# Optimization experiments

Hardware: AMD Instinct MI355X
Metric: run time of the kernel (lower is better)

Reference implementation:

```python
import jax, jax.numpy as jnp
import numpy as np

N_NODES = 50000
N_EDGES = 640000
DIM = 128
N_LAYERS = 4
K_MAX = 4


def setup_inputs() -> dict:
    key = jax.random.key(0)
    k1, k2, k3, k4, k5, k6 = jax.random.split(key, 6)
    x = jax.random.normal(k1, (N_NODES, DIM), dtype=jnp.float32)
    edge_index = jax.random.randint(k2, (2, N_EDGES), 0, N_NODES, dtype=jnp.int32)
    edge_attr = jax.random.randint(k3, (N_EDGES,), 1, K_MAX + 1, dtype=jnp.int32)  # hop k in [1, k_max]
    W = jax.random.normal(k4, (N_LAYERS, DIM, DIM), dtype=jnp.float32) * 0.05
    b = jax.random.normal(k5, (N_LAYERS, DIM), dtype=jnp.float32) * 0.01
    alpha = jax.random.normal(k6, (N_LAYERS, K_MAX), dtype=jnp.float32)
    return {"x": x, "edge_index": edge_index, "edge_attr": edge_attr,
            "W": W, "b": b, "alpha": alpha}


def reference(x, edge_index, edge_attr, W, b, alpha):
    # SP-GCN stage: per-hop GCN convs with shared per-layer weight W[t],
    # combined with softmax(alpha[t]) hop weights, residual + ReLU + L2 norm.
    N, D = x.shape
    L, K = alpha.shape
    src, dst = edge_index[0], edge_index[1]
    k_idx = edge_attr - 1                              # [E] in [0, K)

    # Per-(node, hop) in-degree with self-loop (+1), as in gcn_norm per k-subgraph.
    seg = dst * K + k_idx
    ones = jnp.ones(src.shape[0], dtype=x.dtype)
    deg = jax.ops.segment_sum(ones, seg, num_segments=N * K).reshape(N, K) + 1.0  # [N, K]
    dinv = jax.lax.rsqrt(deg)
    # symmetric norm per edge within its hop-k subgraph
    norm_e = dinv[src, k_idx] * dinv[dst, k_idx]       # [E]

    for t in range(L):
        a = jax.nn.softmax(alpha[t])                   # [K] hop weights
        h = x @ W[t]                                   # [N, D]
        # sum_k alpha_k * conv_k fused: per-edge weight alpha[k_e] * norm_e
        msg = (a[k_idx] * norm_e)[:, None] * h[src]    # [E, D]
        agg = jax.ops.segment_sum(msg, dst, num_segments=N)
        # self-loop contributions: sum_k alpha_k / deg[n, k]
        self_coef = jnp.sum(a[None, :] / deg, axis=1)  # [N]
        out = agg + self_coef[:, None] * h + b[t]
        x = x + jax.nn.relu(out)
        # F.normalize(p=2, dim=-1), eps=1e-12
        nrm = jnp.maximum(jnp.linalg.norm(x, axis=-1, keepdims=True), 1e-12)
        x = x / nrm
    return x
```

## Files before the change

### kernel.cpp

```cpp
#include <hip/hip_runtime.h>
#include <hip/hip_fp16.h>
#include <math.h>

#define DIM 128
#define KH 4

typedef unsigned int uint;
typedef unsigned short ushort;

__global__ __launch_bounds__(256) void k_init(const float4* __restrict__ xin,
                                              float4* __restrict__ X4,
                                              uint* __restrict__ degpack,
                                              int n4, int N) {
  int i = blockIdx.x * 256 + threadIdx.x;
  if (i < n4) X4[i] = xin[i];
  if (i < N) degpack[i] = 0;
}

__global__ __launch_bounds__(256) void k_count(const int* __restrict__ ei,
                                               const int* __restrict__ attr,
                                               uint* __restrict__ degpack, int E) {
  int e = blockIdx.x * 256 + threadIdx.x;
  if (e >= E) return;
  int dst = ei[E + e];
  int k = attr[e] - 1;
  atomicAdd(&degpack[dst], 1u << (k * 8));
}

__global__ __launch_bounds__(256) void k_scan1(const uint* __restrict__ degpack,
                                               int* __restrict__ off,
                                               int* __restrict__ bsum, int n) {
  __shared__ int s[256];
  int t = threadIdx.x;
  int i = blockIdx.x * 256 + t;
  int v = 0;
  if (i < n) {
    uint w = degpack[i];
    v = (w & 0xff) + ((w >> 8) & 0xff) + ((w >> 16) & 0xff) + (w >> 24);
  }
  s[t] = v;
  __syncthreads();
  for (int d = 1; d < 256; d <<= 1) {
    int u = (t >= d) ? s[t - d] : 0;
    __syncthreads();
    s[t] += u;
    __syncthreads();
  }
  if (i < n) off[i] = s[t] - v;
  if (t == 255) bsum[blockIdx.x] = s[255];
}

__global__ __launch_bounds__(256) void k_scan2(const int* __restrict__ bsum,
                                               int* __restrict__ bex, int nb) {
  __shared__ int s[256];
  int t = threadIdx.x;
  int v = (t < nb) ? bsum[t] : 0;
  s[t] = v;
  __syncthreads();
  for (int d = 1; d < 256; d <<= 1) {
    int u = (t >= d) ? s[t - d] : 0;
    __syncthreads();
    s[t] += u;
    __syncthreads();
  }
  if (t < nb) bex[t] = s[t] - v;
}

__global__ __launch_bounds__(256) void k_scan3(int* __restrict__ off,
                                               const int* __restrict__ bex,
                                               const uint* __restrict__ degpack,
                                               int* __restrict__ cursor4,
                                               float* __restrict__ dinv, int n) {
  int i = blockIdx.x * 256 + threadIdx.x;
  if (i >= n) return;
  int o = off[i] + bex[blockIdx.x];
  off[i] = o;
  uint w = degpack[i];
  int b0 = w & 0xff, b1 = (w >> 8) & 0xff, b2 = (w >> 16) & 0xff, b3 = w >> 24;
  int4 c;
  c.x = o;
  c.y = o + b0;
  c.z = o + b0 + b1;
  c.w = o + b0 + b1 + b2;
  *(int4*)&cursor4[i * 4] = c;
  float4 dv;
  dv.x = rsqrtf((float)b0 + 1.0f);
  dv.y = rsqrtf((float)b1 + 1.0f);
  dv.z = rsqrtf((float)b2 + 1.0f);
  dv.w = rsqrtf((float)b3 + 1.0f);
  *(float4*)&dinv[i * 4] = dv;
}

__global__ __launch_bounds__(256) void k_scatter(const int* __restrict__ ei,
                                                 const int* __restrict__ attr,
                                                 const float* __restrict__ dinv,
                                                 int* __restrict__ cursor4,
                                                 uint* __restrict__ srcnm, int E) {
  int e = blockIdx.x * 256 + threadIdx.x;
  if (e >= E) return;
  int src = ei[e];
  int dst = ei[E + e];
  int k = attr[e] - 1;
  float nm = dinv[src * KH + k] * dinv[dst * KH + k];
  ushort h = __half_as_ushort(__float2half(nm));
  int pos = atomicAdd(&cursor4[dst * KH + k], 1);
  srcnm[pos] = (uint)src | ((uint)h << 16);
}

__device__ __forceinline__ uint f2bf(float f) {
  uint u = __float_as_uint(f);
  return (u + 0x7fffu + ((u >> 16) & 1u)) >> 16;
}
__device__ __forceinline__ float bflo(uint u) { return __uint_as_float(u << 16); }
__device__ __forceinline__ float bfhi(uint u) { return __uint_as_float(u & 0xffff0000u); }

#define FMA4(A, xc, wv)                 \
  A.x = fmaf(xc, wv.x, A.x);            \
  A.y = fmaf(xc, wv.y, A.y);            \
  A.z = fmaf(xc, wv.z, A.z);            \
  A.w = fmaf(xc, wv.w, A.w);

__global__ __launch_bounds__(256) void k_gemm(const float* __restrict__ X,
                                              const float* __restrict__ W,
                                              uint* __restrict__ Hb,
                                              int N) {
  __shared__ float xs[64][64];
  __shared__ float ws[64][128];
  int t = threadIdx.x;
  int r0 = blockIdx.x * 64;
  int tc = t & 31;
  int tr = t >> 5;
  float4 acc[8];
#pragma unroll
  for (int i = 0; i < 8; ++i) acc[i] = make_float4(0.f, 0.f, 0.f, 0.f);

  for (int kb = 0; kb < 2; ++kb) {
    __syncthreads();
#pragma unroll
    for (int i = 0; i < 4; ++i) {
      int fi = i * 256 + t;
      int kq = fi & 15, rr = fi >> 4;
      int row = r0 + rr;
      if (row >= N) row = N - 1;
      *(float4*)&xs[rr][kq * 4] =
          *(const float4*)&X[(size_t)row * DIM + kb * 64 + kq * 4];
    }
#pragma unroll
    for (int i = 0; i < 8; ++i) {
      int fi = i * 256 + t;
      int jq = fi & 31, kk = fi >> 5;
      *(float4*)&ws[kk][jq * 4] =
          *(const float4*)&W[(size_t)(kb * 64 + kk) * DIM + jq * 4];
    }
    __syncthreads();
#pragma unroll
    for (int k4 = 0; k4 < 16; ++k4) {
      float4 wv0 = *(float4*)&ws[k4 * 4 + 0][tc * 4];
      float4 wv1 = *(float4*)&ws[k4 * 4 + 1][tc * 4];
      float4 wv2 = *(float4*)&ws[k4 * 4 + 2][tc * 4];
      float4 wv3 = *(float4*)&ws[k4 * 4 + 3][tc * 4];
#pragma unroll
      for (int rr = 0; rr < 8; ++rr) {
        float4 xv = *(float4*)&xs[tr * 8 + rr][k4 * 4];
        FMA4(acc[rr], xv.x, wv0)
        FMA4(acc[rr], xv.y, wv1)
        FMA4(acc[rr], xv.z, wv2)
        FMA4(acc[rr], xv.w, wv3)
      }
    }
  }
#pragma unroll
  for (int rr = 0; rr < 8; ++rr) {
    int row = r0 + tr * 8 + rr;
    if (row < N) {
      uint2 o;
      o.x = f2bf(acc[rr].x) | (f2bf(acc[rr].y) << 16);
      o.y = f2bf(acc[rr].z) | (f2bf(acc[rr].w) << 16);
      *(uint2*)&Hb[(size_t)row * 64 + tc * 2] = o;
    }
  }
}

__global__ __launch_bounds__(256) void k_agg(const int* __restrict__ off,
                                             const uint* __restrict__ degpack,
                                             const uint* __restrict__ srcnm,
                                             const float* __restrict__ dinv,
                                             const uint* __restrict__ Hb,
                                             const float* __restrict__ bias,
                                             const float* __restrict__ alpha,
                                             float* __restrict__ X, int N) {
  int wid = threadIdx.x >> 6;
  int lane = threadIdx.x & 63;
  int n = blockIdx.x * 4 + wid;
  if (n >= N) return;

  float a0 = alpha[0], a1 = alpha[1], a2 = alpha[2], a3 = alpha[3];
  float m = fmaxf(fmaxf(a0, a1), fmaxf(a2, a3));
  a0 = __expf(a0 - m); a1 = __expf(a1 - m); a2 = __expf(a2 - m); a3 = __expf(a3 - m);
  float is = 1.0f / (a0 + a1 + a2 + a3);
  a0 *= is; a1 *= is; a2 *= is; a3 *= is;

  uint w = degpack[n];
  int b0 = w & 0xff, b1 = (w >> 8) & 0xff, b2 = (w >> 16) & 0xff, b3 = (int)(w >> 24);
  int e0 = off[n];
  int e1 = e0 + b0 + b1 + b2 + b3;
  int k1 = e0 + b0, k2 = k1 + b1, k3 = k2 + b2;

  float accx = 0.f, accy = 0.f;

  for (int base = e0; base < e1; base += 64) {
    int cnt = min(64, e1 - base);
    int sofs = 0;
    float wc = 0.f;
    if (lane < cnt) {
      uint v = srcnm[base + lane];
      int pos = base + lane;
      int k = (pos >= k1) + (pos >= k2) + (pos >= k3);
      float ak = (k == 0) ? a0 : (k == 1) ? a1 : (k == 2) ? a2 : a3;
      wc = ak * __half2float(__ushort_as_half((ushort)(v >> 16)));
      sofs = (int)(v & 0xFFFFu) << 6;
    }
    int j = 0;
    for (; j + 4 <= cnt; j += 4) {
      int s0 = __shfl(sofs, j),     s1 = __shfl(sofs, j + 1);
      int s2 = __shfl(sofs, j + 2), s3 = __shfl(sofs, j + 3);
      float w0 = __shfl(wc, j),     w1 = __shfl(wc, j + 1);
      float w2 = __shfl(wc, j + 2), w3 = __shfl(wc, j + 3);
      uint u0 = Hb[s0 + lane];
      uint u1 = Hb[s1 + lane];
      uint u2 = Hb[s2 + lane];
      uint u3 = Hb[s3 + lane];
      accx = fmaf(w0, bflo(u0), accx); accy = fmaf(w0, bfhi(u0), accy);
      accx = fmaf(w1, bflo(u1), accx); accy = fmaf(w1, bfhi(u1), accy);
      accx = fmaf(w2, bflo(u2), accx); accy = fmaf(w2, bfhi(u2), accy);
      accx = fmaf(w3, bflo(u3), accx); accy = fmaf(w3, bfhi(u3), accy);
    }
    for (; j < cnt; ++j) {
      int sj = __shfl(sofs, j);
      float wj = __shfl(wc, j);
      uint uj = Hb[sj + lane];
      accx = fmaf(wj, bflo(uj), accx);
      accy = fmaf(wj, bfhi(uj), accy);
    }
  }

  float4 dv = *(const float4*)&dinv[n * 4];
  float sc = a0 * dv.x * dv.x + a1 * dv.y * dv.y + a2 * dv.z * dv.z + a3 * dv.w * dv.w;

  uint un = Hb[(size_t)n * 64 + lane];
  float2 bb = ((const float2*)bias)[lane];
  float2 xo = ((const float2*)X)[(size_t)n * 64 + lane];
  float o0 = accx + sc * bflo(un) + bb.x;
  float o1 = accy + sc * bfhi(un) + bb.y;
  float x0 = xo.x + fmaxf(o0, 0.f);
  float x1 = xo.y + fmaxf(o1, 0.f);

  float ss = x0 * x0 + x1 * x1;
#pragma unroll
  for (int d = 32; d; d >>= 1) ss += __shfl_xor(ss, d);
  float nrm = fmaxf(sqrtf(ss), 1e-12f);
  float inv = 1.0f / nrm;
  ((float2*)X)[(size_t)n * 64 + lane] = make_float2(x0 * inv, x1 * inv);
}

extern "C" void kernel_launch(void* const* d_in, const int* in_sizes, int n_in,
                              void* d_out, int out_size, void* d_ws, size_t ws_size,
                              hipStream_t stream) {
  const float* x = (const float*)d_in[0];
  const int* ei = (const int*)d_in[1];
  const int* attr = (const int*)d_in[2];
  const float* W = (const float*)d_in[3];
  const float* b = (const float*)d_in[4];
  const float* alpha = (const float*)d_in[5];
  float* X = (float*)d_out;

  int N = in_sizes[0] / DIM;
  int E = in_sizes[1] / 2;
  int L = in_sizes[3] / (DIM * DIM);

  char* base = (char*)d_ws;
  size_t ofs = 0;
  auto carve = [&](size_t bytes) -> void* {
    void* p = base + ofs;
    ofs = (ofs + bytes + 255) & ~(size_t)255;
    return p;
  };
  int* off = (int*)carve((size_t)(N + 1) * 4);
  int* cursor4 = (int*)carve((size_t)N * KH * 4);
  uint* degpack = (uint*)carve((size_t)N * 4);
  float* dinv = (float*)carve((size_t)N * KH * 4);
  int* bsum = (int*)carve(256 * 4);
  int* bex = (int*)carve(256 * 4);
  uint* srcnm = (uint*)carve((size_t)E * 4);
  uint* Hb = (uint*)carve((size_t)N * 64 * 4);

  int n4 = N * DIM / 4;
  int nb = (N + 255) / 256;

  k_init<<<(n4 + 255) / 256, 256, 0, stream>>>((const float4*)x, (float4*)X,
                                               degpack, n4, N);
  k_count<<<(E + 255) / 256, 256, 0, stream>>>(ei, attr, degpack, E);
  k_scan1<<<nb, 256, 0, stream>>>(degpack, off, bsum, N);
  k_scan2<<<1, 256, 0, stream>>>(bsum, bex, nb);
  k_scan3<<<nb, 256, 0, stream>>>(off, bex, degpack, cursor4, dinv, N);
  k_scatter<<<(E + 255) / 256, 256, 0, stream>>>(ei, attr, dinv, cursor4, srcnm, E);

  for (int t = 0; t < L; ++t) {
    k_gemm<<<(N + 63) / 64, 256, 0, stream>>>(X, W + (size_t)t * DIM * DIM, Hb, N);
    k_agg<<<(N + 3) / 4, 256, 0, stream>>>(off, degpack, srcnm, dinv, Hb,
                                           b + (size_t)t * DIM, alpha + (size_t)t * KH,
                                           X, N);
  }
}
```

Baseline: 334.4 us.

## Replace FP32 FMA GEMM with split-bf16 MFMA GEMM using hi/lo operands

```diff
diff --git a/kernel.cpp b/kernel.cpp
--- a/kernel.cpp
+++ b/kernel.cpp
@@ -7,14 +7,53 @@
 
 typedef unsigned int uint;
 typedef unsigned short ushort;
+using short8v = __attribute__((ext_vector_type(8))) short;
+using f32x4 = __attribute__((ext_vector_type(4))) float;
+
+__device__ __forceinline__ uint f2bf(float f) {
+  uint u = __float_as_uint(f);
+  return (u + 0x7fffu + ((u >> 16) & 1u)) >> 16;
+}
+__device__ __forceinline__ float bf2f(uint u) { return __uint_as_float(u << 16); }
+__device__ __forceinline__ float bflo(uint u) { return __uint_as_float(u << 16); }
+__device__ __forceinline__ float bfhi(uint u) { return __uint_as_float(u & 0xffff0000u); }
 
 __global__ __launch_bounds__(256) void k_init(const float4* __restrict__ xin,
                                               float4* __restrict__ X4,
+                                              uint* __restrict__ Xhi,
+                                              uint* __restrict__ Xlo,
                                               uint* __restrict__ degpack,
                                               int n4, int N) {
   int i = blockIdx.x * 256 + threadIdx.x;
-  if (i < n4) X4[i] = xin[i];
+  if (i < n4) {
+    float4 v = xin[i];
+    X4[i] = v;
+    uint h0 = f2bf(v.x), h1 = f2bf(v.y), h2 = f2bf(v.z), h3 = f2bf(v.w);
+    Xhi[i * 2 + 0] = h0 | (h1 << 16);
+    Xhi[i * 2 + 1] = h2 | (h3 << 16);
+    uint l0 = f2bf(v.x - bf2f(h0)), l1 = f2bf(v.y - bf2f(h1));
+    uint l2 = f2bf(v.z - bf2f(h2)), l3 = f2bf(v.w - bf2f(h3));
+    Xlo[i * 2 + 0] = l0 | (l1 << 16);
+    Xlo[i * 2 + 1] = l2 | (l3 << 16);
+  }
   if (i < N) degpack[i] = 0;
+}
+
+__global__ __launch_bounds__(256) void k_wprep(const float* __restrict__ W,
+                                               short* __restrict__ Whi,
+                                               short* __restrict__ Wlo, int total) {
+  int idx = blockIdx.x * 256 + threadIdx.x;
+  if (idx >= total) return;
+  int l = idx >> 14;
+  int rem = idx & 16383;
+  int k = rem >> 7;
+  int n = rem & 127;
+  float w = W[idx];
+  uint h = f2bf(w);
+  uint lo = f2bf(w - bf2f(h));
+  size_t o = (size_t)l * 16384 + (size_t)n * 128 + k;
+  Whi[o] = (short)h;
+  Wlo[o] = (short)lo;
 }
 
 __global__ __launch_bounds__(256) void k_count(const int* __restrict__ ei,
@@ -107,78 +146,77 @@
   srcnm[pos] = (uint)src | ((uint)h << 16);
 }
 
-__device__ __forceinline__ uint f2bf(float f) {
-  uint u = __float_as_uint(f);
-  return (u + 0x7fffu + ((u >> 16) & 1u)) >> 16;
-}
-__device__ __forceinline__ float bflo(uint u) { return __uint_as_float(u << 16); }
-__device__ __forceinline__ float bfhi(uint u) { return __uint_as_float(u & 0xffff0000u); }
-
-#define FMA4(A, xc, wv)                 \
-  A.x = fmaf(xc, wv.x, A.x);            \
-  A.y = fmaf(xc, wv.y, A.y);            \
-  A.z = fmaf(xc, wv.z, A.z);            \
-  A.w = fmaf(xc, wv.w, A.w);
-
-__global__ __launch_bounds__(256) void k_gemm(const float* __restrict__ X,
-                                              const float* __restrict__ W,
-                                              uint* __restrict__ Hb,
-                                              int N) {
-  __shared__ float xs[64][64];
-  __shared__ float ws[64][128];
+__global__ __launch_bounds__(512) void k_gemm(const uint* __restrict__ Xhi,
+                                              const uint* __restrict__ Xlo,
+                                              const short* __restrict__ Whi,
+                                              const short* __restrict__ Wlo,
+                                              ushort* __restrict__ Hb16, int N) {
+  __shared__ __align__(16) short xs_hi[64 * 128];
+  __shared__ __align__(16) short xs_lo[64 * 128];
   int t = threadIdx.x;
   int r0 = blockIdx.x * 64;
-  int tc = t & 31;
-  int tr = t >> 5;
-  float4 acc[8];
-#pragma unroll
-  for (int i = 0; i < 8; ++i) acc[i] = make_float4(0.f, 0.f, 0.f, 0.f);
-
-  for (int kb = 0; kb < 2; ++kb) {
-    __syncthreads();
-#pragma unroll
-    for (int i = 0; i < 4; ++i) {
-      int fi = i * 256 + t;
-      int kq = fi & 15, rr = fi >> 4;
-      int row = r0 + rr;
-      if (row >= N) row = N - 1;
-      *(float4*)&xs[rr][kq * 4] =
-          *(const float4*)&X[(size_t)row * DIM + kb * 64 + kq * 4];
-    }
-#pragma unroll
-    for (int i = 0; i < 8; ++i) {
-      int fi = i * 256 + t;
-      int jq = fi & 31, kk = fi >> 5;
-      *(float4*)&ws[kk][jq * 4] =
-          *(const float4*)&W[(size_t)(kb * 64 + kk) * DIM + jq * 4];
-    }
-    __syncthreads();
-#pragma unroll
-    for (int k4 = 0; k4 < 16; ++k4) {
-      float4 wv0 = *(float4*)&ws[k4 * 4 + 0][tc * 4];
-      float4 wv1 = *(float4*)&ws[k4 * 4 + 1][tc * 4];
-      float4 wv2 = *(float4*)&ws[k4 * 4 + 2][tc * 4];
-      float4 wv3 = *(float4*)&ws[k4 * 4 + 3][tc * 4];
-#pragma unroll
-      for (int rr = 0; rr < 8; ++rr) {
-        float4 xv = *(float4*)&xs[tr * 8 + rr][k4 * 4];
-        FMA4(acc[rr], xv.x, wv0)
-        FMA4(acc[rr], xv.y, wv1)
-        FMA4(acc[rr], xv.z, wv2)
-        FMA4(acc[rr], xv.w, wv3)
+
+#pragma unroll
+  for (int i = 0; i < 2; ++i) {
+    int fi = i * 512 + t;
+    int row = fi >> 4, kq = fi & 15;
+    int rg = r0 + row;
+    if (rg >= N) rg = N - 1;
+    int swz = kq ^ (row & 7);
+    *(uint4*)&xs_hi[row * 128 + swz * 8] = *(const uint4*)&Xhi[(size_t)rg * 64 + kq * 4];
+    *(uint4*)&xs_lo[row * 128 + swz * 8] = *(const uint4*)&Xlo[(size_t)rg * 64 + kq * 4];
+  }
+  __syncthreads();
+
+  int wid = t >> 6, lane = t & 63;
+  int wrow = wid & 1, wcol = wid >> 1;
+  int lr = lane & 15, lk = lane >> 4;
+
+  f32x4 acc[2][2];
+#pragma unroll
+  for (int a = 0; a < 2; ++a)
+#pragma unroll
+    for (int c = 0; c < 2; ++c) acc[a][c] = (f32x4){0.f, 0.f, 0.f, 0.f};
+
+#pragma unroll
+  for (int ks = 0; ks < 4; ++ks) {
+    int k0 = ks * 32 + lk * 8;
+    short8v ah[2], al[2];
+#pragma unroll
+    for (int rt = 0; rt < 2; ++rt) {
+      int r = wrow * 32 + rt * 16 + lr;
+      int slot = (k0 >> 3) ^ (r & 7);
+      ah[rt] = *(short8v*)&xs_hi[r * 128 + slot * 8];
+      al[rt] = *(short8v*)&xs_lo[r * 128 + slot * 8];
+    }
+    short8v bh[2], bl[2];
+#pragma unroll
+    for (int ct = 0; ct < 2; ++ct) {
+      int col = wcol * 32 + ct * 16 + lr;
+      bh[ct] = *(const short8v*)&Whi[(size_t)col * 128 + k0];
+      bl[ct] = *(const short8v*)&Wlo[(size_t)col * 128 + k0];
+    }
+#pragma unroll
+    for (int rt = 0; rt < 2; ++rt)
+#pragma unroll
+      for (int ct = 0; ct < 2; ++ct) {
+        acc[rt][ct] = __builtin_amdgcn_mfma_f32_16x16x32_bf16(ah[rt], bh[ct], acc[rt][ct], 0, 0, 0);
+        acc[rt][ct] = __builtin_amdgcn_mfma_f32_16x16x32_bf16(al[rt], bh[ct], acc[rt][ct], 0, 0, 0);
+        acc[rt][ct] = __builtin_amdgcn_mfma_f32_16x16x32_bf16(ah[rt], bl[ct], acc[rt][ct], 0, 0, 0);
       }
-    }
-  }
-#pragma unroll
-  for (int rr = 0; rr < 8; ++rr) {
-    int row = r0 + tr * 8 + rr;
-    if (row < N) {
-      uint2 o;
-      o.x = f2bf(acc[rr].x) | (f2bf(acc[rr].y) << 16);
-      o.y = f2bf(acc[rr].z) | (f2bf(acc[rr].w) << 16);
-      *(uint2*)&Hb[(size_t)row * 64 + tc * 2] = o;
-    }
-  }
+  }
+
+#pragma unroll
+  for (int rt = 0; rt < 2; ++rt)
+#pragma unroll
+    for (int ct = 0; ct < 2; ++ct) {
+      int col = wcol * 32 + ct * 16 + lr;
+#pragma unroll
+      for (int i = 0; i < 4; ++i) {
+        int row = r0 + wrow * 32 + rt * 16 + lk * 4 + i;
+        if (row < N) Hb16[(size_t)row * 128 + col] = (ushort)f2bf(acc[rt][ct][i]);
+      }
+    }
 }
 
 __global__ __launch_bounds__(256) void k_agg(const int* __restrict__ off,
@@ -188,7 +226,9 @@
                                              const uint* __restrict__ Hb,
                                              const float* __restrict__ bias,
                                              const float* __restrict__ alpha,
-                                             float* __restrict__ X, int N) {
+                                             float* __restrict__ X,
+                                             uint* __restrict__ Xhi,
+                                             uint* __restrict__ Xlo, int N) {
   int wid = threadIdx.x >> 6;
   int lane = threadIdx.x & 63;
   int n = blockIdx.x * 4 + wid;
@@ -260,7 +300,13 @@
   for (int d = 32; d; d >>= 1) ss += __shfl_xor(ss, d);
   float nrm = fmaxf(sqrtf(ss), 1e-12f);
   float inv = 1.0f / nrm;
-  ((float2*)X)[(size_t)n * 64 + lane] = make_float2(x0 * inv, x1 * inv);
+  float y0 = x0 * inv, y1 = x1 * inv;
+  ((float2*)X)[(size_t)n * 64 + lane] = make_float2(y0, y1);
+
+  uint h0 = f2bf(y0), h1 = f2bf(y1);
+  Xhi[(size_t)n * 64 + lane] = h0 | (h1 << 16);
+  uint l0 = f2bf(y0 - bf2f(h0)), l1 = f2bf(y1 - bf2f(h1));
+  Xlo[(size_t)n * 64 + lane] = l0 | (l1 << 16);
 }
 
 extern "C" void kernel_launch(void* const* d_in, const int* in_sizes, int n_in,
@@ -293,22 +339,31 @@
   int* bex = (int*)carve(256 * 4);
   uint* srcnm = (uint*)carve((size_t)E * 4);
   uint* Hb = (uint*)carve((size_t)N * 64 * 4);
+  uint* Xhi = (uint*)carve((size_t)N * 64 * 4);
+  uint* Xlo = (uint*)carve((size_t)N * 64 * 4);
+  short* Whi = (short*)carve((size_t)L * DIM * DIM * 2);
+  short* Wlo = (short*)carve((size_t)L * DIM * DIM * 2);
 
   int n4 = N * DIM / 4;
   int nb = (N + 255) / 256;
+  int wtot = L * DIM * DIM;
 
   k_init<<<(n4 + 255) / 256, 256, 0, stream>>>((const float4*)x, (float4*)X,
-                                               degpack, n4, N);
+                                               Xhi, Xlo, degpack, n4, N);
   k_count<<<(E + 255) / 256, 256, 0, stream>>>(ei, attr, degpack, E);
   k_scan1<<<nb, 256, 0, stream>>>(degpack, off, bsum, N);
   k_scan2<<<1, 256, 0, stream>>>(bsum, bex, nb);
   k_scan3<<<nb, 256, 0, stream>>>(off, bex, degpack, cursor4, dinv, N);
   k_scatter<<<(E + 255) / 256, 256, 0, stream>>>(ei, attr, dinv, cursor4, srcnm, E);
+  k_wprep<<<(wtot + 255) / 256, 256, 0, stream>>>(W, Whi, Wlo, wtot);
 
   for (int t = 0; t < L; ++t) {
-    k_gemm<<<(N + 63) / 64, 256, 0, stream>>>(X, W + (size_t)t * DIM * DIM, Hb, N);
+    k_gemm<<<(N + 63) / 64, 512, 0, stream>>>(Xhi, Xlo,
+                                              Whi + (size_t)t * DIM * DIM,
+                                              Wlo + (size_t)t * DIM * DIM,
+                                              (ushort*)Hb, N);
     k_agg<<<(N + 3) / 4, 256, 0, stream>>>(off, degpack, srcnm, dinv, Hb,
                                            b + (size_t)t * DIM, alpha + (size_t)t * KH,
-                                           X, N);
-  }
-}
+                                           X, Xhi, Xlo, N);
+  }
+}
```

Result: faster. 318.4 us (-4.8%).
